# Kernel optimization log

Measured on AMD Instinct MI355X. Metric: run time of the kernel, lower is better.

Reference implementation:

```python
import jax, jax.numpy as jnp
import numpy as np

B, N, FDIM = 8, 2048, 256
ASSIGN_RATIO = 0.1
K = int(N * ASSIGN_RATIO) + 1  # num coarse nodes per graph (205)
DENSITY = 0.01


def setup_inputs() -> dict:
    key = jax.random.key(0)
    k1, k2, k3 = jax.random.split(key, 3)
    x = jax.random.normal(k1, (B, N, FDIM), dtype=jnp.float32)
    u = jax.random.uniform(k2, (B, N, N), dtype=jnp.float32)
    adj = jnp.where(u < DENSITY, u, 0.0)
    adj = 0.5 * (adj + jnp.swapaxes(adj, 1, 2))  # symmetric weighted adjacency
    W = jax.random.normal(k3, (FDIM, 1), dtype=jnp.float32) * 0.05
    b = jnp.zeros((1,), dtype=jnp.float32)
    return {"x": x, "adj": adj, "W": W, "b": b}


def _coarsen(x, adj, W, b):
    I = jnp.eye(N, dtype=adj.dtype)
    # --- GCNConv attention score (self-loops + symmetric normalization) ---
    A_hat = adj + I                       # [B,N,N]
    dg = A_hat.sum(-1) ** -0.5            # deg >= 1 via self-loop
    gcn_norm = dg[:, :, None] * A_hat * dg[:, None, :]
    alpha = jnp.einsum('bnm,bmf,fo->bno', gcn_norm, x, W) + b
    alpha = jax.nn.sigmoid(alpha ** 2)[..., 0]   # [B,N], sigmoid(gcn^2)
    # --- normalize_batch_adj: D^{-1/2}(A+I)D^{-1/2}, zero isolated rows ---
    d = jnp.clip(A_hat.sum(-1), 1.0, None) ** -0.5
    norm_adj = d[:, :, None] * A_hat * d[:, None, :]
    norm_adj = norm_adj * (adj.sum(-1) > 0).astype(adj.dtype)[:, :, None]
    # --- top-k cut on attention ---
    topv, topi = jax.lax.top_k(alpha, K)  # [B,K]
    cut = topv[:, K - 1]                  # k-th largest value per graph
    cut_alpha = jax.nn.relu(alpha + 1e-7 - cut[:, None])   # [B,N]
    # --- assignment matrix S = L1-row-normalized(norm_adj * cut_alpha_cols) ---
    S = norm_adj * cut_alpha[:, None, :]
    S = S / jnp.clip(jnp.abs(S).sum(-1, keepdims=True), 1e-12, None)
    # --- coarsening matmuls ---
    x_c = jnp.einsum('bnm,bnf->bmf', S, x)                 # S^T x
    coarse = jnp.einsum('bnm,bnk,bkl->bml', S, adj, S)     # S^T A S
    coarse = jnp.floor(coarse * 1e4) / 1e4                 # 4-digit truncation
    return x_c, coarse, S, topi


def reference(x, adj, W, b):
    return _coarsen(x, adj, W, b)
```

## Files before the change

### kernel.cpp

```cpp
#include <hip/hip_runtime.h>
#include <cstdint>
#include <cstddef>

#define BB 8
#define NN 2048
#define FD 256
#define KK 205
#define CAP 96
#define SELCAP 256

__global__ __launch_bounds__(256) void k_spy(const float* __restrict__ adj, const float* __restrict__ x,
                                             const float* __restrict__ W, int* __restrict__ ell_idx,
                                             float* __restrict__ ell_val, int* __restrict__ ell_cnt,
                                             float* __restrict__ dg, float* __restrict__ y) {
  int r = blockIdx.x;
  const float4* arow4 = (const float4*)(adj + (size_t)r * NN);
  int t = threadIdx.x;
  int lane = t & 63, wv = t >> 6;
  __shared__ int counter;
  __shared__ float wsum[4], wy[4];
  if (t == 0) counter = 0;
  __syncthreads();
  size_t base = (size_t)r * CAP;
  float ls = 0.f;
#pragma unroll
  for (int j = 0; j < 2; ++j) {
    int i4 = t + j * 256;
    float4 v = arow4[i4];
    int m0 = i4 * 4;
    if (v.x != 0.f) { int p = atomicAdd(&counter, 1); if (p < CAP) { ell_idx[base + p] = m0 + 0; ell_val[base + p] = v.x; } ls += v.x; }
    if (v.y != 0.f) { int p = atomicAdd(&counter, 1); if (p < CAP) { ell_idx[base + p] = m0 + 1; ell_val[base + p] = v.y; } ls += v.y; }
    if (v.z != 0.f) { int p = atomicAdd(&counter, 1); if (p < CAP) { ell_idx[base + p] = m0 + 2; ell_val[base + p] = v.z; } ls += v.z; }
    if (v.w != 0.f) { int p = atomicAdd(&counter, 1); if (p < CAP) { ell_idx[base + p] = m0 + 3; ell_val[base + p] = v.w; } ls += v.w; }
  }
#pragma unroll
  for (int off = 32; off > 0; off >>= 1) ls += __shfl_down(ls, off);
  if (lane == 0) wsum[wv] = ls;
  float xv = x[(size_t)r * FD + t] * W[t];
#pragma unroll
  for (int off = 32; off > 0; off >>= 1) xv += __shfl_down(xv, off);
  if (lane == 0) wy[wv] = xv;
  __syncthreads();
  if (t == 0) {
    int tot = counter; if (tot > CAP) tot = CAP;
    ell_cnt[r] = tot;
    float rs = wsum[0] + wsum[1] + wsum[2] + wsum[3];
    dg[r] = 1.0f / sqrtf(1.0f + rs);
    y[r] = wy[0] + wy[1] + wy[2] + wy[3];
  }
}

__global__ __launch_bounds__(256) void k_alpha(const int* __restrict__ ell_idx, const float* __restrict__ ell_val,
                                               const int* __restrict__ ell_cnt, const float* __restrict__ dg,
                                               const float* __restrict__ y, const float* __restrict__ bptr,
                                               float* __restrict__ alpha) {
  int lane = threadIdx.x & 63, wv = threadIdx.x >> 6;
  int r = blockIdx.x * 4 + wv;
  int b = r / NN;
  int cnt = ell_cnt[r];
  size_t base = (size_t)r * CAP;
  const float* dgb = dg + (size_t)b * NN;
  const float* yb = y + (size_t)b * NN;
  float acc = 0.f;
  for (int j = lane; j < cnt; j += 64) {
    int m = ell_idx[base + j];
    acc += ell_val[base + j] * dgb[m] * yb[m];
  }
#pragma unroll
  for (int off = 32; off > 0; off >>= 1) acc += __shfl_down(acc, off);
  if (lane == 0) {
    float dgn = dg[r];
    float z = dgn * (acc + dgn * y[r]) + bptr[0];
    float t2 = z * z;
    alpha[r] = 1.0f / (1.0f + expf(-t2));
  }
}

__global__ __launch_bounds__(256) void k_rank(const float* __restrict__ alpha, float* __restrict__ cutv,
                                              float* __restrict__ out_topi, int* __restrict__ sel_cnt) {
  __shared__ unsigned int keys[NN];
  int b = blockIdx.x & 7;
  int chunk = blockIdx.x >> 3;
  int t = threadIdx.x;
  if (chunk == 0 && t == 0) sel_cnt[b] = 0;
  const float* ab = alpha + (size_t)b * NN;
  for (int i = t; i < NN; i += 256) keys[i] = __float_as_uint(ab[i]);
  __syncthreads();
  int i = chunk * 256 + t;
  unsigned int ai = keys[i];
  int rank = 0;
  const uint4* k4 = (const uint4*)keys;
#pragma unroll 4
  for (int j4 = 0; j4 < NN / 4; ++j4) {
    uint4 v = k4[j4];
    int j = j4 * 4;
    rank += (v.x > ai) || (v.x == ai && (j + 0) < i);
    rank += (v.y > ai) || (v.y == ai && (j + 1) < i);
    rank += (v.z > ai) || (v.z == ai && (j + 2) < i);
    rank += (v.w > ai) || (v.w == ai && (j + 3) < i);
  }
  if (rank < KK) out_topi[(size_t)b * KK + rank] = (float)i;
  if (rank == KK - 1) cutv[b] = __uint_as_float(ai);
}

__global__ __launch_bounds__(256) void k_selcut(const float* __restrict__ alpha, const float* __restrict__ cutv,
                                                float* __restrict__ cutA, int* __restrict__ selidx,
                                                int* __restrict__ sel_list, int* __restrict__ sel_cnt) {
  int r = blockIdx.x * 256 + threadIdx.x;
  int b = r / NN, n = r % NN;
  float ca = fmaxf(alpha[r] + 1e-7f - cutv[b], 0.0f);
  cutA[r] = ca;
  int s = -1;
  if (ca > 0.f) {
    s = atomicAdd(&sel_cnt[b], 1);
    if (s < SELCAP) sel_list[b * SELCAP + s] = n; else s = -1;
  }
  selidx[r] = s;
}

__global__ __launch_bounds__(256) void k_sbuild(const int* __restrict__ ell_idx, const float* __restrict__ ell_val,
                                                const int* __restrict__ ell_cnt, const float* __restrict__ dg,
                                                const float* __restrict__ cutA, const int* __restrict__ selidx,
                                                float* __restrict__ inv_eff,
                                                float* __restrict__ Sc, float* __restrict__ outS) {
  __shared__ float row[NN];
  __shared__ float scrow[SELCAP];
  __shared__ int   sidx[CAP];
  __shared__ float sterm[CAP];
  __shared__ float wred[4];
  __shared__ float s_inv, s_dv;
  int r = blockIdx.x;
  int b = r >> 11;
  int t = threadIdx.x;
  int lane = t & 63, wv = t >> 6;
#pragma unroll
  for (int j = 0; j < NN / 256; ++j) row[t + j * 256] = 0.f;
  if (t < SELCAP) scrow[t] = 0.f;
  int cnt = ell_cnt[r];
  size_t base = (size_t)r * CAP;
  float dgn = dg[r];
  const float* dgb = dg + (size_t)b * NN;
  const float* cab = cutA + (size_t)b * NN;
  const int* sib = selidx + (size_t)b * NN;
  float part = 0.f;
  for (int j = t; j < cnt; j += 256) {
    int m = ell_idx[base + j];
    float term = dgn * ell_val[base + j] * dgb[m] * cab[m];
    sidx[j] = m; sterm[j] = term;
    part += term;
  }
#pragma unroll
  for (int off = 32; off > 0; off >>= 1) part += __shfl_down(part, off);
  if (lane == 0) wred[wv] = part;
  __syncthreads();
  if (t == 0) {
    float diag = dgn * dgn * cutA[r];
    float rho = wred[0] + wred[1] + wred[2] + wred[3] + diag;
    float inv = (cnt > 0) ? (1.0f / fmaxf(rho, 1e-12f)) : 0.f;
    s_inv = inv; s_dv = diag * inv;
    inv_eff[r] = inv;
  }
  __syncthreads();
  float inv = s_inv;
  for (int j = t; j < cnt; j += 256) {
    float v = sterm[j] * inv;
    row[sidx[j]] = v;
    int si = sib[sidx[j]];
    if (si >= 0) scrow[si] = v;
  }
  __syncthreads();
  if (t == 0) {
    int n = r & (NN - 1);
    row[n] += s_dv;
    int si = sib[n];
    if (si >= 0) scrow[si] += s_dv;
  }
  __syncthreads();
  float4* dst = (float4*)(outS + (size_t)r * NN);
  const float4* src = (const float4*)row;
#pragma unroll
  for (int j = 0; j < NN / 4 / 256; ++j) dst[t + j * 256] = src[t + j * 256];
  if (t < SELCAP) Sc[(size_t)r * SELCAP + t] = scrow[t];
}

__global__ __launch_bounds__(256) void k_M(const int* __restrict__ ell_idx, const float* __restrict__ ell_val,
                                           const int* __restrict__ ell_cnt, const float* __restrict__ Sc,
                                           float* __restrict__ Mmat) {
  int b = blockIdx.x & 7;
  int n = blockIdx.x >> 3;
  int r = b * NN + n;
  int t = threadIdx.x;
  __shared__ int srk[CAP];
  __shared__ float sav[CAP];
  int cnt = ell_cnt[r];
  size_t base = (size_t)r * CAP;
  for (int e = t; e < cnt; e += 256) {
    srk[e] = b * NN + ell_idx[base + e];
    sav[e] = ell_val[base + e];
  }
  __syncthreads();
  float a0 = 0.f;
  for (int e = 0; e < cnt; ++e) a0 += sav[e] * Sc[(size_t)srk[e] * SELCAP + t];
  Mmat[(size_t)r * SELCAP + t] = a0;
}

__global__ __launch_bounds__(256) void k_epi2(const float* __restrict__ x, const int* __restrict__ ell_idx,
                                              const float* __restrict__ ell_val, const int* __restrict__ ell_cnt,
                                              const float* __restrict__ dg, const float* __restrict__ cutA,
                                              const float* __restrict__ inv_eff, const int* __restrict__ selidx,
                                              const int* __restrict__ sel_list, const int* __restrict__ sel_cnt,
                                              const float* __restrict__ Mmat,
                                              float* __restrict__ xc, float* __restrict__ coarse) {
  int b = blockIdx.x & 7;
  int m = blockIdx.x >> 3;
  int rm = b * NN + m;
  int t = threadIdx.x;
  __shared__ float row[NN];
  __shared__ int cn[CAP + 1];
  __shared__ float cw[CAP + 1];
#pragma unroll
  for (int j = 0; j < NN / 256; ++j) row[t + j * 256] = 0.f;
  bool sel = selidx[rm] >= 0;
  int nsel = sel_cnt[b]; if (nsel > SELCAP) nsel = SELCAP;
  int cnt = ell_cnt[rm];
  if (sel) {
    float dgm = dg[rm], cam = cutA[rm];
    for (int j = t; j <= cnt; j += 256) {
      if (j < cnt) {
        int n = ell_idx[(size_t)rm * CAP + j];
        cn[j] = b * NN + n;
        cw[j] = ell_val[(size_t)rm * CAP + j] * dg[b * NN + n] * dgm * cam * inv_eff[b * NN + n];
      } else {
        cn[j] = rm;
        cw[j] = dgm * dgm * cam * inv_eff[rm];
      }
    }
  }
  __syncthreads();
  float axc = 0.f;
  if (sel) {
    float aco = 0.f;
    for (int e = 0; e <= cnt; ++e) {
      float w = cw[e];
      if (w == 0.f) continue;
      size_t rn = (size_t)cn[e];
      axc += w * x[rn * FD + t];
      aco += w * Mmat[rn * SELCAP + t];
    }
    if (t < nsel) row[sel_list[b * SELCAP + t]] = floorf(aco * 10000.0f) / 10000.0f;
  }
  xc[(size_t)rm * FD + t] = axc;
  __syncthreads();
  float4* dst = (float4*)(coarse + (size_t)rm * NN);
  const float4* src = (const float4*)row;
#pragma unroll
  for (int j = 0; j < NN / 4 / 256; ++j) dst[t + j * 256] = src[t + j * 256];
}

extern "C" void kernel_launch(void* const* d_in, const int* in_sizes, int n_in,
                              void* d_out, int out_size, void* d_ws, size_t ws_size,
                              hipStream_t stream) {
  (void)in_sizes; (void)n_in; (void)ws_size; (void)out_size;
  const float* x = (const float*)d_in[0];
  const float* adj = (const float*)d_in[1];
  const float* W = (const float*)d_in[2];
  const float* bptr = (const float*)d_in[3];

  float* out = (float*)d_out;
  const size_t XC_SZ = (size_t)BB * NN * FD;
  const size_t CO_SZ = (size_t)BB * NN * NN;
  const size_t S_SZ  = (size_t)BB * NN * NN;
  float* out_xc = out;
  float* out_co = out + XC_SZ;
  float* out_S  = out + XC_SZ + CO_SZ;
  float* out_ti = out + XC_SZ + CO_SZ + S_SZ;

  char* w = (char*)d_ws;
  int*   ell_idx = (int*)w;   w += (size_t)BB * NN * CAP * 4;
  float* ell_val = (float*)w; w += (size_t)BB * NN * CAP * 4;
  float* Sc      = (float*)w; w += (size_t)BB * NN * SELCAP * 4;
  float* Mmat    = (float*)w; w += (size_t)BB * NN * SELCAP * 4;
  int*   ell_cnt = (int*)w;   w += (size_t)BB * NN * 4;
  float* dg      = (float*)w; w += (size_t)BB * NN * 4;
  float* yv      = (float*)w; w += (size_t)BB * NN * 4;
  float* alpha   = (float*)w; w += (size_t)BB * NN * 4;
  float* cutA    = (float*)w; w += (size_t)BB * NN * 4;
  float* inv_eff = (float*)w; w += (size_t)BB * NN * 4;
  int*   selidx  = (int*)w;   w += (size_t)BB * NN * 4;
  float* cutv    = (float*)w; w += (size_t)BB * 4;
  int*   sel_cnt = (int*)w;   w += (size_t)BB * 4;
  int*   sel_list= (int*)w;   w += (size_t)BB * SELCAP * 4;

  k_spy<<<BB * NN, 256, 0, stream>>>(adj, x, W, ell_idx, ell_val, ell_cnt, dg, yv);
  k_alpha<<<BB * NN / 4, 256, 0, stream>>>(ell_idx, ell_val, ell_cnt, dg, yv, bptr, alpha);
  k_rank<<<BB * 8, 256, 0, stream>>>(alpha, cutv, out_ti, sel_cnt);
  k_selcut<<<BB * NN / 256, 256, 0, stream>>>(alpha, cutv, cutA, selidx, sel_list, sel_cnt);
  k_sbuild<<<BB * NN, 256, 0, stream>>>(ell_idx, ell_val, ell_cnt, dg, cutA, selidx,
                                        inv_eff, Sc, out_S);
  k_M<<<BB * NN, 256, 0, stream>>>(ell_idx, ell_val, ell_cnt, Sc, Mmat);
  k_epi2<<<BB * NN, 256, 0, stream>>>(x, ell_idx, ell_val, ell_cnt, dg, cutA, inv_eff,
                                      selidx, sel_list, sel_cnt, Mmat, out_xc, out_co);
}
```

Before: 544.4 us.

## Pack ELL idx/val into int2, use wave-ballot compaction, early-exit unselected rows

Stores ELL column index and value together as int2 so each edge needs one 8-byte load instead of two separate loads. k_spy replaces per-element shared atomics with a wave ballot plus popcount prefix, so there is one atomic per wave per component. k_M uses four independent accumulators to expose more memory-level parallelism. k_epi2 lets rows that are not selected write zeros with float4 stores and return before the shared-memory setup and gather loop. The ELL write order changes, which can alter floating-point summation order.

```diff
diff --git a/kernel.cpp b/kernel.cpp
--- a/kernel.cpp
+++ b/kernel.cpp
@@ -9,10 +9,11 @@
 #define CAP 96
 #define SELCAP 256
 
+
 __global__ __launch_bounds__(256) void k_spy(const float* __restrict__ adj, const float* __restrict__ x,
-                                             const float* __restrict__ W, int* __restrict__ ell_idx,
-                                             float* __restrict__ ell_val, int* __restrict__ ell_cnt,
-                                             float* __restrict__ dg, float* __restrict__ y) {
+                                             const float* __restrict__ W, int2* __restrict__ ell,
+                                             int* __restrict__ ell_cnt, float* __restrict__ dg,
+                                             float* __restrict__ y) {
   int r = blockIdx.x;
   const float4* arow4 = (const float4*)(adj + (size_t)r * NN);
   int t = threadIdx.x;
@@ -22,16 +23,29 @@
   if (t == 0) counter = 0;
   __syncthreads();
   size_t base = (size_t)r * CAP;
+  unsigned long long lmask = (1ull << lane) - 1;
   float ls = 0.f;
 #pragma unroll
   for (int j = 0; j < 2; ++j) {
     int i4 = t + j * 256;
     float4 v = arow4[i4];
     int m0 = i4 * 4;
-    if (v.x != 0.f) { int p = atomicAdd(&counter, 1); if (p < CAP) { ell_idx[base + p] = m0 + 0; ell_val[base + p] = v.x; } ls += v.x; }
-    if (v.y != 0.f) { int p = atomicAdd(&counter, 1); if (p < CAP) { ell_idx[base + p] = m0 + 1; ell_val[base + p] = v.y; } ls += v.y; }
-    if (v.z != 0.f) { int p = atomicAdd(&counter, 1); if (p < CAP) { ell_idx[base + p] = m0 + 2; ell_val[base + p] = v.z; } ls += v.z; }
-    if (v.w != 0.f) { int p = atomicAdd(&counter, 1); if (p < CAP) { ell_idx[base + p] = m0 + 3; ell_val[base + p] = v.w; } ls += v.w; }
+    float vv[4] = {v.x, v.y, v.z, v.w};
+#pragma unroll
+    for (int c = 0; c < 4; ++c) {
+      float val = vv[c];
+      unsigned long long mk = __ballot(val != 0.f);
+      if (mk) {
+        int wbase = 0;
+        if (lane == 0) wbase = atomicAdd(&counter, (int)__popcll(mk));
+        wbase = __shfl(wbase, 0);
+        if (val != 0.f) {
+          int p = wbase + (int)__popcll(mk & lmask);
+          if (p < CAP) ell[base + p] = make_int2(m0 + c, __float_as_int(val));
+        }
+      }
+      ls += val;
+    }
   }
 #pragma unroll
   for (int off = 32; off > 0; off >>= 1) ls += __shfl_down(ls, off);
@@ -50,10 +64,9 @@
   }
 }
 
-__global__ __launch_bounds__(256) void k_alpha(const int* __restrict__ ell_idx, const float* __restrict__ ell_val,
-                                               const int* __restrict__ ell_cnt, const float* __restrict__ dg,
-                                               const float* __restrict__ y, const float* __restrict__ bptr,
-                                               float* __restrict__ alpha) {
+__global__ __launch_bounds__(256) void k_alpha(const int2* __restrict__ ell, const int* __restrict__ ell_cnt,
+                                               const float* __restrict__ dg, const float* __restrict__ y,
+                                               const float* __restrict__ bptr, float* __restrict__ alpha) {
   int lane = threadIdx.x & 63, wv = threadIdx.x >> 6;
   int r = blockIdx.x * 4 + wv;
   int b = r / NN;
@@ -63,8 +76,8 @@
   const float* yb = y + (size_t)b * NN;
   float acc = 0.f;
   for (int j = lane; j < cnt; j += 64) {
-    int m = ell_idx[base + j];
-    acc += ell_val[base + j] * dgb[m] * yb[m];
+    int2 e = ell[base + j];
+    acc += __int_as_float(e.y) * dgb[e.x] * yb[e.x];
   }
 #pragma unroll
   for (int off = 32; off > 0; off >>= 1) acc += __shfl_down(acc, off);
@@ -118,10 +131,9 @@
   selidx[r] = s;
 }
 
-__global__ __launch_bounds__(256) void k_sbuild(const int* __restrict__ ell_idx, const float* __restrict__ ell_val,
-                                                const int* __restrict__ ell_cnt, const float* __restrict__ dg,
-                                                const float* __restrict__ cutA, const int* __restrict__ selidx,
-                                                float* __restrict__ inv_eff,
+__global__ __launch_bounds__(256) void k_sbuild(const int2* __restrict__ ell, const int* __restrict__ ell_cnt,
+                                                const float* __restrict__ dg, const float* __restrict__ cutA,
+                                                const int* __restrict__ selidx, float* __restrict__ inv_eff,
                                                 float* __restrict__ Sc, float* __restrict__ outS) {
   __shared__ float row[NN];
   __shared__ float scrow[SELCAP];
@@ -144,9 +156,9 @@
   const int* sib = selidx + (size_t)b * NN;
   float part = 0.f;
   for (int j = t; j < cnt; j += 256) {
-    int m = ell_idx[base + j];
-    float term = dgn * ell_val[base + j] * dgb[m] * cab[m];
-    sidx[j] = m; sterm[j] = term;
+    int2 e = ell[base + j];
+    float term = dgn * __int_as_float(e.y) * dgb[e.x] * cab[e.x];
+    sidx[j] = e.x; sterm[j] = term;
     part += term;
   }
 #pragma unroll
@@ -183,9 +195,8 @@
   if (t < SELCAP) Sc[(size_t)r * SELCAP + t] = scrow[t];
 }
 
-__global__ __launch_bounds__(256) void k_M(const int* __restrict__ ell_idx, const float* __restrict__ ell_val,
-                                           const int* __restrict__ ell_cnt, const float* __restrict__ Sc,
-                                           float* __restrict__ Mmat) {
+__global__ __launch_bounds__(256) void k_M(const int2* __restrict__ ell, const int* __restrict__ ell_cnt,
+                                           const float* __restrict__ Sc, float* __restrict__ Mmat) {
   int b = blockIdx.x & 7;
   int n = blockIdx.x >> 3;
   int r = b * NN + n;
@@ -195,21 +206,28 @@
   int cnt = ell_cnt[r];
   size_t base = (size_t)r * CAP;
   for (int e = t; e < cnt; e += 256) {
-    srk[e] = b * NN + ell_idx[base + e];
-    sav[e] = ell_val[base + e];
-  }
-  __syncthreads();
-  float a0 = 0.f;
-  for (int e = 0; e < cnt; ++e) a0 += sav[e] * Sc[(size_t)srk[e] * SELCAP + t];
-  Mmat[(size_t)r * SELCAP + t] = a0;
-}
-
-__global__ __launch_bounds__(256) void k_epi2(const float* __restrict__ x, const int* __restrict__ ell_idx,
-                                              const float* __restrict__ ell_val, const int* __restrict__ ell_cnt,
-                                              const float* __restrict__ dg, const float* __restrict__ cutA,
-                                              const float* __restrict__ inv_eff, const int* __restrict__ selidx,
-                                              const int* __restrict__ sel_list, const int* __restrict__ sel_cnt,
-                                              const float* __restrict__ Mmat,
+    int2 p = ell[base + e];
+    srk[e] = b * NN + p.x;
+    sav[e] = __int_as_float(p.y);
+  }
+  __syncthreads();
+  float a0 = 0.f, a1 = 0.f, a2 = 0.f, a3 = 0.f;
+  int e = 0;
+  for (; e + 4 <= cnt; e += 4) {
+    a0 += sav[e + 0] * Sc[(size_t)srk[e + 0] * SELCAP + t];
+    a1 += sav[e + 1] * Sc[(size_t)srk[e + 1] * SELCAP + t];
+    a2 += sav[e + 2] * Sc[(size_t)srk[e + 2] * SELCAP + t];
+    a3 += sav[e + 3] * Sc[(size_t)srk[e + 3] * SELCAP + t];
+  }
+  for (; e < cnt; ++e) a0 += sav[e] * Sc[(size_t)srk[e] * SELCAP + t];
+  Mmat[(size_t)r * SELCAP + t] = (a0 + a1) + (a2 + a3);
+}
+
+__global__ __launch_bounds__(256) void k_epi2(const float* __restrict__ x, const int2* __restrict__ ell,
+                                              const int* __restrict__ ell_cnt, const float* __restrict__ dg,
+                                              const float* __restrict__ cutA, const float* __restrict__ inv_eff,
+                                              const int* __restrict__ selidx, const int* __restrict__ sel_list,
+                                              const int* __restrict__ sel_cnt, const float* __restrict__ Mmat,
                                               float* __restrict__ xc, float* __restrict__ coarse) {
   int b = blockIdx.x & 7;
   int m = blockIdx.x >> 3;
@@ -218,18 +236,26 @@
   __shared__ float row[NN];
   __shared__ int cn[CAP + 1];
   __shared__ float cw[CAP + 1];
-#pragma unroll
-  for (int j = 0; j < NN / 256; ++j) row[t + j * 256] = 0.f;
   bool sel = selidx[rm] >= 0;
+  if (!sel) {
+    float4 z = make_float4(0.f, 0.f, 0.f, 0.f);
+    if (t < FD / 4) ((float4*)(xc + (size_t)rm * FD))[t] = z;
+    float4* dco = (float4*)(coarse + (size_t)rm * NN);
+    dco[t] = z;
+    dco[t + 256] = z;
+    return;
+  }
   int nsel = sel_cnt[b]; if (nsel > SELCAP) nsel = SELCAP;
   int cnt = ell_cnt[rm];
-  if (sel) {
+#pragma unroll
+  for (int j = 0; j < NN / 256; ++j) row[t + j * 256] = 0.f;
+  {
     float dgm = dg[rm], cam = cutA[rm];
     for (int j = t; j <= cnt; j += 256) {
       if (j < cnt) {
-        int n = ell_idx[(size_t)rm * CAP + j];
-        cn[j] = b * NN + n;
-        cw[j] = ell_val[(size_t)rm * CAP + j] * dg[b * NN + n] * dgm * cam * inv_eff[b * NN + n];
+        int2 e = ell[(size_t)rm * CAP + j];
+        cn[j] = b * NN + e.x;
+        cw[j] = __int_as_float(e.y) * dg[b * NN + e.x] * dgm * cam * inv_eff[b * NN + e.x];
       } else {
         cn[j] = rm;
         cw[j] = dgm * dgm * cam * inv_eff[rm];
@@ -237,18 +263,15 @@
     }
   }
   __syncthreads();
-  float axc = 0.f;
-  if (sel) {
-    float aco = 0.f;
-    for (int e = 0; e <= cnt; ++e) {
-      float w = cw[e];
-      if (w == 0.f) continue;
-      size_t rn = (size_t)cn[e];
-      axc += w * x[rn * FD + t];
-      aco += w * Mmat[rn * SELCAP + t];
-    }
-    if (t < nsel) row[sel_list[b * SELCAP + t]] = floorf(aco * 10000.0f) / 10000.0f;
-  }
+  float axc = 0.f, aco = 0.f;
+  for (int e = 0; e <= cnt; ++e) {
+    float w = cw[e];
+    if (w == 0.f) continue;
+    size_t rn = (size_t)cn[e];
+    axc += w * x[rn * FD + t];
+    aco += w * Mmat[rn * SELCAP + t];
+  }
+  if (t < nsel) row[sel_list[b * SELCAP + t]] = floorf(aco * 10000.0f) / 10000.0f;
   xc[(size_t)rm * FD + t] = axc;
   __syncthreads();
   float4* dst = (float4*)(coarse + (size_t)rm * NN);
@@ -276,8 +299,7 @@
   float* out_ti = out + XC_SZ + CO_SZ + S_SZ;
 
   char* w = (char*)d_ws;
-  int*   ell_idx = (int*)w;   w += (size_t)BB * NN * CAP * 4;
-  float* ell_val = (float*)w; w += (size_t)BB * NN * CAP * 4;
+  int2*  ell     = (int2*)w;  w += (size_t)BB * NN * CAP * 8;
   float* Sc      = (float*)w; w += (size_t)BB * NN * SELCAP * 4;
   float* Mmat    = (float*)w; w += (size_t)BB * NN * SELCAP * 4;
   int*   ell_cnt = (int*)w;   w += (size_t)BB * NN * 4;
@@ -291,13 +313,12 @@
   int*   sel_cnt = (int*)w;   w += (size_t)BB * 4;
   int*   sel_list= (int*)w;   w += (size_t)BB * SELCAP * 4;
 
-  k_spy<<<BB * NN, 256, 0, stream>>>(adj, x, W, ell_idx, ell_val, ell_cnt, dg, yv);
-  k_alpha<<<BB * NN / 4, 256, 0, stream>>>(ell_idx, ell_val, ell_cnt, dg, yv, bptr, alpha);
+  k_spy<<<BB * NN, 256, 0, stream>>>(adj, x, W, ell, ell_cnt, dg, yv);
+  k_alpha<<<BB * NN / 4, 256, 0, stream>>>(ell, ell_cnt, dg, yv, bptr, alpha);
   k_rank<<<BB * 8, 256, 0, stream>>>(alpha, cutv, out_ti, sel_cnt);
   k_selcut<<<BB * NN / 256, 256, 0, stream>>>(alpha, cutv, cutA, selidx, sel_list, sel_cnt);
-  k_sbuild<<<BB * NN, 256, 0, stream>>>(ell_idx, ell_val, ell_cnt, dg, cutA, selidx,
-                                        inv_eff, Sc, out_S);
-  k_M<<<BB * NN, 256, 0, stream>>>(ell_idx, ell_val, ell_cnt, Sc, Mmat);
-  k_epi2<<<BB * NN, 256, 0, stream>>>(x, ell_idx, ell_val, ell_cnt, dg, cutA, inv_eff,
+  k_sbuild<<<BB * NN, 256, 0, stream>>>(ell, ell_cnt, dg, cutA, selidx, inv_eff, Sc, out_S);
+  k_M<<<BB * NN, 256, 0, stream>>>(ell, ell_cnt, Sc, Mmat);
+  k_epi2<<<BB * NN, 256, 0, stream>>>(x, ell, ell_cnt, dg, cutA, inv_eff,
                                       selidx, sel_list, sel_cnt, Mmat, out_xc, out_co);
 }
```

New measurement: 538.0 us. No clear change (-1.2%).
